# Kernel optimization log

Measured on AMD Instinct MI355X. Metric: run time of the kernel, lower is better.

The kernel has to match this reference:

```python
import jax, jax.numpy as jnp
import numpy as np

NA, NP, NT = 100000, 200000, 50000      # authors, papers, terms
DA, DP, DT = 128, 128, 64               # input feature dims per node type
E_AP, E_PA, E_TP, E_PT = 400000, 400000, 300000, 300000
H, OUT = 64, 4                          # hidden_channels, out_channels
NEG_SLOPE = 0.01                        # nn.LeakyReLU default


def setup_inputs() -> dict:
    keys = iter(jax.random.split(jax.random.key(0), 64))
    rn = lambda shape, s=0.05: jax.random.normal(next(keys), shape, dtype=jnp.float32) * s
    ri = lambda n, hi: jax.random.randint(next(keys), (n,), 0, hi, dtype=jnp.int32)
    inp = {
        'x_author': rn((NA, DA), 1.0),
        'x_paper': rn((NP, DP), 1.0),
        'x_term': rn((NT, DT), 1.0),
        'src_ap': ri(E_AP, NA), 'dst_ap': ri(E_AP, NP),
        'src_pa': ri(E_PA, NP), 'dst_pa': ri(E_PA, NA),
        'src_tp': ri(E_TP, NT), 'dst_tp': ri(E_TP, NP),
        'src_pt': ri(E_PT, NP), 'dst_pt': ri(E_PT, NT),
    }
    # SAGEConv params per edge type: Wl (on mean-aggregated src feats, with bias),
    # Wr (root/dst feats, no bias) -- matches PyG SAGEConv(lin_l, lin_r).
    dims = {'ap': (DA, DP), 'pa': (DP, DA), 'tp': (DT, DP), 'pt': (DP, DT)}
    for et, (ds, dd) in dims.items():
        inp['l1_' + et + '_Wl'] = rn((ds, H))
        inp['l1_' + et + '_bl'] = rn((H,))
        inp['l1_' + et + '_Wr'] = rn((dd, H))
        inp['l2_' + et + '_Wl'] = rn((H, H))
        inp['l2_' + et + '_bl'] = rn((H,))
        inp['l2_' + et + '_Wr'] = rn((H, H))
    inp['lin_W'] = rn((H, OUT))
    inp['lin_b'] = rn((OUT,))
    return inp


def _sage(x_src, x_dst, src, dst, Wl, bl, Wr):
    """PyG SAGEConv (mean aggr): lin_l(mean_j x_src[j]) + lin_r(x_dst)."""
    n_dst = x_dst.shape[0]
    agg = jax.ops.segment_sum(x_src[src], dst, num_segments=n_dst)        # [n_dst, d_src]
    cnt = jax.ops.segment_sum(jnp.ones_like(dst, dtype=x_src.dtype), dst, num_segments=n_dst)
    mean = agg / jnp.maximum(cnt, 1.0)[:, None]
    return mean @ Wl + bl + x_dst @ Wr


def reference(x_author, x_paper, x_term,
              src_ap, dst_ap, src_pa, dst_pa, src_tp, dst_tp, src_pt, dst_pt,
              l1_ap_Wl, l1_ap_bl, l1_ap_Wr, l1_pa_Wl, l1_pa_bl, l1_pa_Wr,
              l1_tp_Wl, l1_tp_bl, l1_tp_Wr, l1_pt_Wl, l1_pt_bl, l1_pt_Wr,
              l2_ap_Wl, l2_ap_bl, l2_ap_Wr, l2_pa_Wl, l2_pa_bl, l2_pa_Wr,
              l2_tp_Wl, l2_tp_bl, l2_tp_Wr, l2_pt_Wl, l2_pt_bl, l2_pt_Wr,
              lin_W, lin_b):
    lrelu = lambda v: jax.nn.leaky_relu(v, NEG_SLOPE)
    # Layer 1 (HeteroConv, sum across relations into each dst type) + LeakyReLU.
    p1 = lrelu(_sage(x_author, x_paper, src_ap, dst_ap, l1_ap_Wl, l1_ap_bl, l1_ap_Wr)
               + _sage(x_term, x_paper, src_tp, dst_tp, l1_tp_Wl, l1_tp_bl, l1_tp_Wr))
    a1 = lrelu(_sage(x_paper, x_author, src_pa, dst_pa, l1_pa_Wl, l1_pa_bl, l1_pa_Wr))
    # (term output of layer 1 / layer-2 paper & term outputs do not reach the
    # returned 'author' logits -- omitted, exactly as autograd would prune them.)
    # Layer 2: author output only needs paper->author relation.
    a2 = _sage(p1, a1, src_pa, dst_pa, l2_pa_Wl, l2_pa_bl, l2_pa_Wr)
    return a2 @ lin_W + lin_b  # [NA, OUT]
```

## Files before the change

### kernel.cpp

```cpp
#include <hip/hip_runtime.h>

#define NA 100000
#define NP 200000
#define NT 50000
#define E_AP 400000
#define E_PA 400000
#define E_TP 300000
#define E_TOT (E_AP + E_TP + E_PA)
#define HD 64
#define NOUT 4
#define NEG 0.01f
#define M_CNT (2 * NP + NA)
#define SCAN_NB ((M_CNT + 1023) / 1024)

typedef __attribute__((ext_vector_type(8))) short bf16x8;
typedef __attribute__((ext_vector_type(4))) float f32x4;

static __device__ __forceinline__ short f2bf(float f) {
  unsigned u = __float_as_uint(f);
  unsigned r = (u + 0x7FFFu + ((u >> 16) & 1u)) >> 16;
  return (short)r;
}
static __device__ __forceinline__ float bflo(unsigned u) {
  return __uint_as_float(u << 16);
}
static __device__ __forceinline__ float bfhi(unsigned u) {
  return __uint_as_float(u & 0xFFFF0000u);
}

static __device__ __forceinline__ void acc8(float* acc, uint4 u, float w) {
  acc[0] = fmaf(w, bflo(u.x), acc[0]);
  acc[1] = fmaf(w, bfhi(u.x), acc[1]);
  acc[2] = fmaf(w, bflo(u.y), acc[2]);
  acc[3] = fmaf(w, bfhi(u.y), acc[3]);
  acc[4] = fmaf(w, bflo(u.z), acc[4]);
  acc[5] = fmaf(w, bfhi(u.z), acc[5]);
  acc[6] = fmaf(w, bflo(u.w), acc[6]);
  acc[7] = fmaf(w, bfhi(u.w), acc[7]);
}

#define R_NP 16384
#define R_NA 32768
#define R_TP 36864
#define R_BLC 36928
#define R_WFL 37184
#define R_WFR 37440
#define R_BF 37444
#define BZ_NB ((M_CNT / 4 + 255) / 256)
__global__ __launch_bounds__(256) void build_zero_kernel(
    const float* __restrict__ l1_ap_Wl, const float* __restrict__ l1_ap_bl,
    const float* __restrict__ l1_ap_Wr,
    const float* __restrict__ l1_pa_Wl, const float* __restrict__ l1_pa_bl,
    const float* __restrict__ l1_pa_Wr,
    const float* __restrict__ l1_tp_Wl, const float* __restrict__ l1_tp_bl,
    const float* __restrict__ l1_tp_Wr,
    const float* __restrict__ l2_Wl, const float* __restrict__ l2_bl,
    const float* __restrict__ l2_Wr,
    const float* __restrict__ lin_W, const float* __restrict__ lin_b,
    short* __restrict__ Wt_np, short* __restrict__ Wt_na, short* __restrict__ Wt_tp,
    float* __restrict__ blc, float* __restrict__ Wfl, float* __restrict__ Wfr,
    float* __restrict__ bf, int* __restrict__ cnt) {
  int t = blockIdx.x * 256 + threadIdx.x;
  int z4 = t * 4;
  if (z4 < M_CNT) *(int4*)(cnt + z4) = make_int4(0, 0, 0, 0);

  if (t < R_NP) {
    int c = t >> 7, k = t & 127;
    float v = (c < 64) ? l1_pa_Wl[k * 64 + c]
                       : (l1_ap_Wr[k * 64 + (c - 64)] + l1_tp_Wr[k * 64 + (c - 64)]);
    Wt_np[t] = f2bf(v);
  } else if (t < R_NA) {
    int i = t - R_NP;
    int c = i >> 7, k = i & 127;
    float v = (c < 64) ? l1_ap_Wl[k * 64 + c] : l1_pa_Wr[k * 64 + (c - 64)];
    Wt_na[i] = f2bf(v);
  } else if (t < R_TP) {
    int i = t - R_NA;
    int c = i >> 6, k = i & 63;
    Wt_tp[i] = f2bf(l1_tp_Wl[k * 64 + c]);
  } else if (t < R_BLC) {
    int c = t - R_TP;
    blc[c] = l1_ap_bl[c] + l1_tp_bl[c];
  } else if (t < R_WFL) {
    int i = t - R_BLC;
    int k = i >> 2, c = i & 3;
    float s = 0.f;
    for (int j = 0; j < HD; ++j) s += l2_Wl[k * HD + j] * lin_W[j * NOUT + c];
    Wfl[i] = s;
  } else if (t < R_WFR) {
    int i = t - R_WFL;
    int k = i >> 2, c = i & 3;
    float s = 0.f;
    for (int j = 0; j < HD; ++j) s += l2_Wr[k * HD + j] * lin_W[j * NOUT + c];
    Wfr[i] = s;
  } else if (t < R_BF) {
    int c = t - R_WFR;
    float s = lin_b[c];
    for (int j = 0; j < HD; ++j) s += l2_bl[j] * lin_W[j * NOUT + c];
    bf[c] = s;
  }
}

__global__ __launch_bounds__(256) void scan1(const int* __restrict__ cnt,
                                             int* __restrict__ offs,
                                             int* __restrict__ bsum) {
  __shared__ int ts[256];
  int t = threadIdx.x;
  int idx = blockIdx.x * 1024 + t * 4;
  int4 v = make_int4(0, 0, 0, 0);
  if (idx < M_CNT) v = *(const int4*)(cnt + idx);
  int s = v.x + v.y + v.z + v.w;
  ts[t] = s;
  __syncthreads();
  for (int off = 1; off < 256; off <<= 1) {
    int a = (t >= off) ? ts[t - off] : 0;
    __syncthreads();
    ts[t] += a;
    __syncthreads();
  }
  int excl = ts[t] - s;
  if (idx < M_CNT) {
    int4 o;
    o.x = excl; o.y = o.x + v.x; o.z = o.y + v.y; o.w = o.z + v.z;
    *(int4*)(offs + idx) = o;
  }
  if (t == 255) bsum[blockIdx.x] = ts[255];
}

__global__ __launch_bounds__(256) void scan2(int* __restrict__ bsum, int nb) {
  __shared__ int ts[256];
  __shared__ int carrysh;
  int t = threadIdx.x;
  int carry = 0;
  for (int base = 0; base < nb; base += 256) {
    int v = (base + t < nb) ? bsum[base + t] : 0;
    ts[t] = v;
    __syncthreads();
    for (int off = 1; off < 256; off <<= 1) {
      int a = (t >= off) ? ts[t - off] : 0;
      __syncthreads();
      ts[t] += a;
      __syncthreads();
    }
    if (base + t < nb) bsum[base + t] = carry + ts[t] - v;
    if (t == 255) carrysh = ts[255];
    __syncthreads();
    carry += carrysh;
    __syncthreads();
  }
}

template <int K, int COLS, bool HAS_OUT1>
static __device__ __forceinline__ void gemm_body(const float* __restrict__ X,
                                                 const short* __restrict__ Wt,
                                                 const float* __restrict__ bias1,
                                                 unsigned short* __restrict__ out0,
                                                 unsigned short* __restrict__ out1,
                                                 int N, int bid,
                                                 unsigned short* __restrict__ lds) {
  constexpr int NSTEP = K / 32;
  constexpr int NTILE = COLS / 16;
  constexpr int WROWB = K * 2;
  constexpr int WBYTES = COLS * K * 2;
  const int t = threadIdx.x;
  const int lane = t & 63;
  const int w = t >> 6;
  const int m = lane & 15;
  const int quad = lane >> 4;

  const int r0 = bid * 128 + w * 16;
  const int r1 = r0 + 64;
  bf16x8 a0[NSTEP], a1[NSTEP];
  {
    const float* x0 = X + (size_t)min(r0 + m, N - 1) * K + quad * 8;
    const float* x1 = X + (size_t)min(r1 + m, N - 1) * K + quad * 8;
#pragma unroll
    for (int s = 0; s < NSTEP; ++s) {
      float4 v0 = *(const float4*)(x0 + s * 32);
      float4 v1 = *(const float4*)(x0 + s * 32 + 4);
      float4 u0 = *(const float4*)(x1 + s * 32);
      float4 u1 = *(const float4*)(x1 + s * 32 + 4);
      bf16x8 a;
      a[0] = f2bf(v0.x); a[1] = f2bf(v0.y); a[2] = f2bf(v0.z); a[3] = f2bf(v0.w);
      a[4] = f2bf(v1.x); a[5] = f2bf(v1.y); a[6] = f2bf(v1.z); a[7] = f2bf(v1.w);
      a0[s] = a;
      bf16x8 b;
      b[0] = f2bf(u0.x); b[1] = f2bf(u0.y); b[2] = f2bf(u0.z); b[3] = f2bf(u0.w);
      b[4] = f2bf(u1.x); b[5] = f2bf(u1.y); b[6] = f2bf(u1.z); b[7] = f2bf(u1.w);
      a1[s] = b;
    }
  }

  {
    const char* wsrc = (const char*)Wt;
    char* wdst = (char*)lds;
#pragma unroll
    for (int i = 0; i < WBYTES / 4096; ++i) {
      const int byte = t * 16 + i * 4096;
      const uint4 v = *(const uint4*)(wsrc + byte);
      const int row = byte / WROWB;
      *(uint4*)(wdst + (byte ^ ((row & 7) << 4))) = v;
    }
  }
  __syncthreads();

  f32x4 acc0[NTILE], acc1[NTILE];
#pragma unroll
  for (int ct = 0; ct < NTILE; ++ct) {
    acc0[ct] = (f32x4){0.f, 0.f, 0.f, 0.f};
    acc1[ct] = (f32x4){0.f, 0.f, 0.f, 0.f};
  }
#pragma unroll
  for (int ct = 0; ct < NTILE; ++ct) {
    const int wrow = ct * 16 + m;
    const int swx = (wrow & 7) << 4;
#pragma unroll
    for (int s = 0; s < NSTEP; ++s) {
      const int byte = wrow * WROWB + s * 64 + quad * 16;
      const bf16x8 b = *(const bf16x8*)((const char*)lds + (byte ^ swx));
      acc0[ct] = __builtin_amdgcn_mfma_f32_16x16x32_bf16(a0[s], b, acc0[ct], 0, 0, 0);
      acc1[ct] = __builtin_amdgcn_mfma_f32_16x16x32_bf16(a1[s], b, acc1[ct], 0, 0, 0);
    }
  }
  __syncthreads();

  constexpr int OROWB = COLS * 2;
#pragma unroll
  for (int ct = 0; ct < NTILE; ++ct) {
    const int col = ct * 16 + m;
    const float add = (HAS_OUT1 && ct >= NTILE / 2) ? bias1[col - 64] : 0.f;
#pragma unroll
    for (int rg = 0; rg < 4; ++rg) {
      const int lr0 = w * 16 + quad * 4 + rg;
      const int lr1 = lr0 + 64;
      const int b0 = lr0 * OROWB + col * 2;
      const int b1 = lr1 * OROWB + col * 2;
      *(unsigned short*)((char*)lds + (b0 ^ ((lr0 & 7) << 4))) =
          (unsigned short)f2bf(acc0[ct][rg] + add);
      *(unsigned short*)((char*)lds + (b1 ^ ((lr1 & 7) << 4))) =
          (unsigned short)f2bf(acc1[ct][rg] + add);
    }
  }
  __syncthreads();

  constexpr int OUTB = 128 * OROWB;
#pragma unroll
  for (int i = 0; i < OUTB / 4096; ++i) {
    const int byte = t * 16 + i * 4096;
    const int row = byte / OROWB;
    const int colb = byte - row * OROWB;
    const uint4 v = *(const uint4*)((const char*)lds + (byte ^ ((row & 7) << 4)));
    const int grow = bid * 128 + row;
    if (grow < N) {
      unsigned short* dst = (HAS_OUT1 && colb >= 128) ? out1 : out0;
      *(uint4*)((char*)dst + (size_t)grow * (HD * 2) + (colb & 127)) = v;
    }
  }
}

#define GB_P ((NP + 127) / 128)
#define GB_A ((NA + 127) / 128)
#define GB_T ((NT + 127) / 128)
#define CNT_NB ((E_TOT / 4 + 255) / 256)

__global__ __launch_bounds__(256, 4) void count_gemm_ta(
    const int* __restrict__ dst_ap, const int* __restrict__ dst_tp,
    const int* __restrict__ dst_pa, int* __restrict__ cnt,
    const float* __restrict__ x_author, const float* __restrict__ x_term,
    const short* __restrict__ Wt_na, const short* __restrict__ Wt_tp,
    const float* __restrict__ l1_pa_bl,
    unsigned short* __restrict__ ya, unsigned short* __restrict__ A1root,
    unsigned short* __restrict__ yt) {
  __shared__ unsigned short lds[16384];
  int b = blockIdx.x;
  if (b < CNT_NB) {
    int i4 = (b * 256 + threadIdx.x) * 4;
    const int* p;
    int base;
    if (i4 < E_AP) { p = dst_ap + i4; base = 0; }
    else if (i4 < E_AP + E_TP) { p = dst_tp + (i4 - E_AP); base = NP; }
    else if (i4 < E_TOT) { p = dst_pa + (i4 - E_AP - E_TP); base = 2 * NP; }
    else return;
    int4 d = *(const int4*)p;
    atomicAdd(&cnt[base + d.x], 1);
    atomicAdd(&cnt[base + d.y], 1);
    atomicAdd(&cnt[base + d.z], 1);
    atomicAdd(&cnt[base + d.w], 1);
  } else if (b < CNT_NB + GB_A) {
    gemm_body<128, 128, true>(x_author, Wt_na, l1_pa_bl, ya, A1root, NA, b - CNT_NB, lds);
  } else {
    gemm_body<64, 64, false>(x_term, Wt_tp, nullptr, yt, nullptr, NT,
                             b - CNT_NB - GB_A, lds);
  }
}

__global__ __launch_bounds__(256, 4) void bucket_gemm_p(
    const int* __restrict__ src_ap, const int* __restrict__ dst_ap,
    const int* __restrict__ src_tp, const int* __restrict__ dst_tp,
    const int* __restrict__ src_pa, const int* __restrict__ dst_pa,
    int* __restrict__ offs, const int* __restrict__ bsum, int* __restrict__ ebuf,
    const float* __restrict__ x_paper, const short* __restrict__ Wt_np,
    const float* __restrict__ blc,
    unsigned short* __restrict__ yp, unsigned short* __restrict__ P1root) {
  __shared__ unsigned short lds[16384];
  int b = blockIdx.x;
  if (b < CNT_NB) {
    int i4 = (b * 256 + threadIdx.x) * 4;
    const int *sp, *dp;
    int base;
    if (i4 < E_AP) { sp = src_ap + i4; dp = dst_ap + i4; base = 0; }
    else if (i4 < E_AP + E_TP) { int j = i4 - E_AP; sp = src_tp + j; dp = dst_tp + j; base = NP; }
    else if (i4 < E_TOT) { int j = i4 - E_AP - E_TP; sp = src_pa + j; dp = dst_pa + j; base = 2 * NP; }
    else return;
    int4 s = *(const int4*)sp;
    int4 d = *(const int4*)dp;
    int gx = base + d.x, gy = base + d.y, gz = base + d.z, gw = base + d.w;
    ebuf[atomicAdd(&offs[gx], 1) + bsum[gx >> 10]] = s.x;
    ebuf[atomicAdd(&offs[gy], 1) + bsum[gy >> 10]] = s.y;
    ebuf[atomicAdd(&offs[gz], 1) + bsum[gz >> 10]] = s.z;
    ebuf[atomicAdd(&offs[gw], 1) + bsum[gw >> 10]] = s.w;
  } else {
    gemm_body<128, 128, true>(x_paper, Wt_np, blc, yp, P1root, NP, b - CNT_NB, lds);
  }
}

__global__ __launch_bounds__(256) void paper_agg(
    const unsigned short* __restrict__ ya, const unsigned short* __restrict__ yt,
    const unsigned short* __restrict__ P1root,
    const int* __restrict__ cnt, const int* __restrict__ offs,
    const int* __restrict__ bsum,
    const int* __restrict__ ebuf, const float* __restrict__ Wfl,
    float* __restrict__ z) {
  const int wv = threadIdx.x >> 6;
  const int lane = threadIdx.x & 63;
  const int g = lane >> 3;
  const int l = lane & 7;
  const int p = blockIdx.x * 32 + wv * 8 + g;
  const bool pv = p < NP;
  const int pc = pv ? p : NP - 1;

  const int cA = cnt[pc], cT = cnt[NP + pc];
  const int startA = offs[pc] + bsum[pc >> 10] - cA;
  const int startT = offs[NP + pc] + bsum[(NP + pc) >> 10] - cT;

  const unsigned short* yab = ya + 8 * l;
  const unsigned short* ytb = yt + 8 * l;

  float accA[8], accT[8];
#pragma unroll
  for (int j = 0; j < 8; ++j) { accA[j] = 0.f; accT[j] = 0.f; }

  const int mx = max(cA, cT);
  for (int i = 0; i < mx; i += 2) {
    const bool a0 = i < cA, a1 = i + 1 < cA;
    const bool t0 = i < cT, t1 = i + 1 < cT;
    int sA0 = ebuf[startA + i];
    int sA1 = ebuf[startA + i + 1];
    int sT0 = ebuf[startT + i];
    int sT1 = ebuf[startT + i + 1];
    sA0 = a0 ? sA0 : 0;
    sA1 = a1 ? sA1 : 0;
    sT0 = t0 ? sT0 : 0;
    sT1 = t1 ? sT1 : 0;
    const uint4 uA0 = *(const uint4*)(yab + (size_t)sA0 * HD);
    const uint4 uA1 = *(const uint4*)(yab + (size_t)sA1 * HD);
    const uint4 uT0 = *(const uint4*)(ytb + (size_t)sT0 * HD);
    const uint4 uT1 = *(const uint4*)(ytb + (size_t)sT1 * HD);
    acc8(accA, uA0, a0 ? 1.f : 0.f);
    acc8(accA, uA1, a1 ? 1.f : 0.f);
    acc8(accT, uT0, t0 ? 1.f : 0.f);
    acc8(accT, uT1, t1 ? 1.f : 0.f);
  }

  const float rA = 1.0f / (float)max(cA, 1);
  const float rT = 1.0f / (float)max(cT, 1);
  uint4 rt = *(const uint4*)(P1root + (size_t)pc * HD + 8 * l);
  float v[8];
  v[0] = bflo(rt.x); v[1] = bfhi(rt.x); v[2] = bflo(rt.y); v[3] = bfhi(rt.y);
  v[4] = bflo(rt.z); v[5] = bfhi(rt.z); v[6] = bflo(rt.w); v[7] = bfhi(rt.w);
  float4 pz = make_float4(0.f, 0.f, 0.f, 0.f);
#pragma unroll
  for (int j = 0; j < 8; ++j) {
    float x = v[j] + accA[j] * rA + accT[j] * rT;
    x = fmaxf(x, NEG * x);
    float4 wf = *(const float4*)(Wfl + (8 * l + j) * 4);
    pz.x += x * wf.x; pz.y += x * wf.y; pz.z += x * wf.z; pz.w += x * wf.w;
  }
#pragma unroll
  for (int m = 1; m < 8; m <<= 1) {
    pz.x += __shfl_xor(pz.x, m);
    pz.y += __shfl_xor(pz.y, m);
    pz.z += __shfl_xor(pz.z, m);
    pz.w += __shfl_xor(pz.w, m);
  }
  if (l == 0 && pv) *(float4*)(z + (size_t)p * NOUT) = pz;
}

__global__ __launch_bounds__(256) void author_agg(
    const unsigned short* __restrict__ yp, const unsigned short* __restrict__ A1root,
    const float* __restrict__ z,
    const int* __restrict__ cnt, const int* __restrict__ offs,
    const int* __restrict__ bsum,
    const int* __restrict__ ebuf, const float* __restrict__ Wfr,
    const float* __restrict__ bf, float* __restrict__ out) {
  const int wv = threadIdx.x >> 6;
  const int lane = threadIdx.x & 63;
  const int g = lane >> 3;
  const int l = lane & 7;
  const int a = blockIdx.x * 32 + wv * 8 + g;
  const bool av = a < NA;
  const int ac = av ? a : NA - 1;

  const int gidx = 2 * NP + ac;
  const int c = cnt[gidx];
  const int start = offs[gidx] + bsum[gidx >> 10] - c;

  const unsigned short* ypb = yp + 8 * l;

  float acc[8];
#pragma unroll
  for (int j = 0; j < 8; ++j) acc[j] = 0.f;
  float4 az = make_float4(0.f, 0.f, 0.f, 0.f);

  for (int i = 0; i < c; i += 2) {
    const bool b1 = i + 1 < c;
    int s0 = ebuf[start + i];
    int s1 = ebuf[min(start + i + 1, E_TOT - 1)];
    s1 = b1 ? s1 : 0;
    const uint4 u0 = *(const uint4*)(ypb + (size_t)s0 * HD);
    const uint4 u1 = *(const uint4*)(ypb + (size_t)s1 * HD);
    const float4 z0 = *(const float4*)(z + (size_t)s0 * NOUT);
    const float4 z1 = *(const float4*)(z + (size_t)s1 * NOUT);
    const float w1 = b1 ? 1.f : 0.f;
    acc8(acc, u0, 1.f);
    acc8(acc, u1, w1);
    az.x = fmaf(w1, z1.x, az.x + z0.x);
    az.y = fmaf(w1, z1.y, az.y + z0.y);
    az.z = fmaf(w1, z1.z, az.z + z0.z);
    az.w = fmaf(w1, z1.w, az.w + z0.w);
  }

  const float r = 1.0f / (float)max(c, 1);
  uint4 rt = *(const uint4*)(A1root + (size_t)ac * HD + 8 * l);
  float v[8];
  v[0] = bflo(rt.x); v[1] = bfhi(rt.x); v[2] = bflo(rt.y); v[3] = bfhi(rt.y);
  v[4] = bflo(rt.z); v[5] = bfhi(rt.z); v[6] = bflo(rt.w); v[7] = bfhi(rt.w);
  float4 o = make_float4(0.f, 0.f, 0.f, 0.f);
#pragma unroll
  for (int j = 0; j < 8; ++j) {
    float x = v[j] + acc[j] * r;
    x = fmaxf(x, NEG * x);
    float4 wf = *(const float4*)(Wfr + (8 * l + j) * 4);
    o.x += x * wf.x; o.y += x * wf.y; o.z += x * wf.z; o.w += x * wf.w;
  }
#pragma unroll
  for (int m = 1; m < 8; m <<= 1) {
    o.x += __shfl_xor(o.x, m);
    o.y += __shfl_xor(o.y, m);
    o.z += __shfl_xor(o.z, m);
    o.w += __shfl_xor(o.w, m);
  }
  if (l == 0 && av) {
    float4 b = *(const float4*)bf;
    o.x += az.x * r + b.x;
    o.y += az.y * r + b.y;
    o.z += az.z * r + b.z;
    o.w += az.w * r + b.w;
    *(float4*)(out + (size_t)a * NOUT) = o;
  }
}

extern "C" void kernel_launch(void* const* d_in, const int* in_sizes, int n_in,
                              void* d_out, int out_size, void* d_ws, size_t ws_size,
                              hipStream_t stream) {
  const float* x_author = (const float*)d_in[0];
  const float* x_paper  = (const float*)d_in[1];
  const float* x_term   = (const float*)d_in[2];
  const int* src_ap = (const int*)d_in[3];
  const int* dst_ap = (const int*)d_in[4];
  const int* src_pa = (const int*)d_in[5];
  const int* dst_pa = (const int*)d_in[6];
  const int* src_tp = (const int*)d_in[7];
  const int* dst_tp = (const int*)d_in[8];
  const float* l1_ap_Wl = (const float*)d_in[11];
  const float* l1_ap_bl = (const float*)d_in[12];
  const float* l1_ap_Wr = (const float*)d_in[13];
  const float* l1_pa_Wl = (const float*)d_in[17];
  const float* l1_pa_bl = (const float*)d_in[18];
  const float* l1_pa_Wr = (const float*)d_in[19];
  const float* l2_pa_Wl = (const float*)d_in[20];
  const float* l2_pa_bl = (const float*)d_in[21];
  const float* l2_pa_Wr = (const float*)d_in[22];
  const float* l1_tp_Wl = (const float*)d_in[23];
  const float* l1_tp_bl = (const float*)d_in[24];
  const float* l1_tp_Wr = (const float*)d_in[25];
  const float* lin_W = (const float*)d_in[35];
  const float* lin_b = (const float*)d_in[36];
  float* out = (float*)d_out;

  char* wsb = (char*)d_ws;
  auto carve = [&](size_t bytes) {
    char* p = wsb;
    wsb += (bytes + 15) & ~(size_t)15;
    return p;
  };
  unsigned short* ya = (unsigned short*)carve((size_t)NA * HD * 2);
  unsigned short* yp = (unsigned short*)carve((size_t)NP * HD * 2);
  unsigned short* yt = (unsigned short*)carve((size_t)NT * HD * 2);
  unsigned short* P1root = (unsigned short*)carve((size_t)NP * HD * 2);
  unsigned short* A1root = (unsigned short*)carve((size_t)NA * HD * 2);
  float* z = (float*)carve((size_t)NP * NOUT * 4);
  int* cnt = (int*)carve((size_t)M_CNT * 4);
  int* offs = (int*)carve((size_t)M_CNT * 4);
  int* bsum = (int*)carve((size_t)SCAN_NB * 4);
  int* ebuf = (int*)carve((size_t)E_TOT * 4);
  short* Wt_np = (short*)carve(128 * 128 * 2);
  short* Wt_na = (short*)carve(128 * 128 * 2);
  short* Wt_tp = (short*)carve(64 * 64 * 2);
  float* blc = (float*)carve(HD * 4);
  float* Wfl = (float*)carve(HD * NOUT * 4);
  float* Wfr = (float*)carve(HD * NOUT * 4);
  float* bf  = (float*)carve(NOUT * 4);

  build_zero_kernel<<<BZ_NB, 256, 0, stream>>>(
      l1_ap_Wl, l1_ap_bl, l1_ap_Wr, l1_pa_Wl, l1_pa_bl, l1_pa_Wr,
      l1_tp_Wl, l1_tp_bl, l1_tp_Wr, l2_pa_Wl, l2_pa_bl, l2_pa_Wr,
      lin_W, lin_b, Wt_np, Wt_na, Wt_tp, blc, Wfl, Wfr, bf, cnt);

  count_gemm_ta<<<CNT_NB + GB_A + GB_T, 256, 0, stream>>>(
      dst_ap, dst_tp, dst_pa, cnt, x_author, x_term, Wt_na, Wt_tp, l1_pa_bl,
      ya, A1root, yt);

  scan1<<<SCAN_NB, 256, 0, stream>>>(cnt, offs, bsum);
  scan2<<<1, 256, 0, stream>>>(bsum, SCAN_NB);

  bucket_gemm_p<<<CNT_NB + GB_P, 256, 0, stream>>>(
      src_ap, dst_ap, src_tp, dst_tp, src_pa, dst_pa, offs, bsum, ebuf,
      x_paper, Wt_np, blc, yp, P1root);

  paper_agg<<<(NP + 31) / 32, 256, 0, stream>>>(ya, yt, P1root, cnt, offs, bsum, ebuf, Wfl, z);
  author_agg<<<(NA + 31) / 32, 256, 0, stream>>>(yp, A1root, z, cnt, offs, bsum, ebuf, Wfr, bf, out);
}
```

Measured before the change: 454.5 us.

## Two-pass binned edge bucketing to localize CSR scatter atomics

Replaces the single-pass random scatter of edges into CSR order with a two-pass scheme. Edges are first coarsely binned by destination range (4096 nodes per bin) using LDS-aggregated bin counters. A second kernel then scatters each bin's edges into ebuf, so atomics and writes stay within a small, cache-resident range. It adds an extra 8-byte-per-edge buffer round trip and a kernel launch, and falls back to the old path if workspace is too small.

After: 480.6 us. +5.7%, slower.

```diff
diff --git a/kernel.cpp b/kernel.cpp
--- a/kernel.cpp
+++ b/kernel.cpp
@@ -12,6 +12,9 @@
 #define NEG 0.01f
 #define M_CNT (2 * NP + NA)
 #define SCAN_NB ((M_CNT + 1023) / 1024)
+#define BINSZ 4096
+#define NBIN ((M_CNT + BINSZ - 1) / BINSZ)
+#define SBPB 8
 
 typedef __attribute__((ext_vector_type(8))) short bf16x8;
 typedef __attribute__((ext_vector_type(4))) float f32x4;
@@ -59,10 +62,11 @@
     const float* __restrict__ lin_W, const float* __restrict__ lin_b,
     short* __restrict__ Wt_np, short* __restrict__ Wt_na, short* __restrict__ Wt_tp,
     float* __restrict__ blc, float* __restrict__ Wfl, float* __restrict__ Wfr,
-    float* __restrict__ bf, int* __restrict__ cnt) {
+    float* __restrict__ bf, int* __restrict__ cnt, int* __restrict__ bincnt) {
   int t = blockIdx.x * 256 + threadIdx.x;
   int z4 = t * 4;
   if (z4 < M_CNT) *(int4*)(cnt + z4) = make_int4(0, 0, 0, 0);
+  if (t < NBIN) bincnt[t] = 0;
 
   if (t < R_NP) {
     int c = t >> 7, k = t & 127;
@@ -127,7 +131,10 @@
   if (t == 255) bsum[blockIdx.x] = ts[255];
 }
 
-__global__ __launch_bounds__(256) void scan2(int* __restrict__ bsum, int nb) {
+__global__ __launch_bounds__(256) void scan2(int* __restrict__ bsum, int nb,
+                                             const int* __restrict__ bincnt,
+                                             int* __restrict__ binoff,
+                                             int* __restrict__ binpos) {
   __shared__ int ts[256];
   __shared__ int carrysh;
   int t = threadIdx.x;
@@ -147,6 +154,20 @@
     __syncthreads();
     carry += carrysh;
     __syncthreads();
+  }
+  int bv = (t < NBIN) ? bincnt[t] : 0;
+  ts[t] = bv;
+  __syncthreads();
+  for (int off = 1; off < 256; off <<= 1) {
+    int a = (t >= off) ? ts[t - off] : 0;
+    __syncthreads();
+    ts[t] += a;
+    __syncthreads();
+  }
+  if (t < NBIN) {
+    int excl = ts[t] - bv;
+    binoff[t] = excl;
+    binpos[t] = excl;
   }
 }
 
@@ -263,9 +284,22 @@
 #define GB_T ((NT + 127) / 128)
 #define CNT_NB ((E_TOT / 4 + 255) / 256)
 
+static __device__ __forceinline__ bool edge_chunk(int i4,
+    const int* __restrict__ src_ap, const int* __restrict__ dst_ap,
+    const int* __restrict__ src_tp, const int* __restrict__ dst_tp,
+    const int* __restrict__ src_pa, const int* __restrict__ dst_pa,
+    const int** sp, const int** dp, int* base) {
+  if (i4 < E_AP) { *sp = src_ap + i4; *dp = dst_ap + i4; *base = 0; return true; }
+  if (i4 < E_AP + E_TP) { int j = i4 - E_AP; *sp = src_tp + j; *dp = dst_tp + j; *base = NP; return true; }
+  if (i4 < E_TOT) { int j = i4 - E_AP - E_TP; *sp = src_pa + j; *dp = dst_pa + j; *base = 2 * NP; return true; }
+  return false;
+}
+
 __global__ __launch_bounds__(256, 4) void count_gemm_ta(
-    const int* __restrict__ dst_ap, const int* __restrict__ dst_tp,
-    const int* __restrict__ dst_pa, int* __restrict__ cnt,
+    const int* __restrict__ src_ap, const int* __restrict__ dst_ap,
+    const int* __restrict__ src_tp, const int* __restrict__ dst_tp,
+    const int* __restrict__ src_pa, const int* __restrict__ dst_pa,
+    int* __restrict__ cnt, int* __restrict__ bincnt,
     const float* __restrict__ x_author, const float* __restrict__ x_term,
     const short* __restrict__ Wt_na, const short* __restrict__ Wt_tp,
     const float* __restrict__ l1_pa_bl,
@@ -274,23 +308,94 @@
   __shared__ unsigned short lds[16384];
   int b = blockIdx.x;
   if (b < CNT_NB) {
+    int* lbin = (int*)lds;
+    for (int i = threadIdx.x; i < NBIN; i += 256) lbin[i] = 0;
+    __syncthreads();
     int i4 = (b * 256 + threadIdx.x) * 4;
-    const int* p;
+    const int *sp, *dp;
     int base;
-    if (i4 < E_AP) { p = dst_ap + i4; base = 0; }
-    else if (i4 < E_AP + E_TP) { p = dst_tp + (i4 - E_AP); base = NP; }
-    else if (i4 < E_TOT) { p = dst_pa + (i4 - E_AP - E_TP); base = 2 * NP; }
-    else return;
-    int4 d = *(const int4*)p;
-    atomicAdd(&cnt[base + d.x], 1);
-    atomicAdd(&cnt[base + d.y], 1);
-    atomicAdd(&cnt[base + d.z], 1);
-    atomicAdd(&cnt[base + d.w], 1);
+    if (edge_chunk(i4, src_ap, dst_ap, src_tp, dst_tp, src_pa, dst_pa, &sp, &dp, &base)) {
+      int4 d = *(const int4*)dp;
+      int gx = base + d.x, gy = base + d.y, gz = base + d.z, gw = base + d.w;
+      atomicAdd(&cnt[gx], 1); atomicAdd(&lbin[gx >> 12], 1);
+      atomicAdd(&cnt[gy], 1); atomicAdd(&lbin[gy >> 12], 1);
+      atomicAdd(&cnt[gz], 1); atomicAdd(&lbin[gz >> 12], 1);
+      atomicAdd(&cnt[gw], 1); atomicAdd(&lbin[gw >> 12], 1);
+    }
+    __syncthreads();
+    for (int i = threadIdx.x; i < NBIN; i += 256)
+      if (lbin[i]) atomicAdd(&bincnt[i], lbin[i]);
   } else if (b < CNT_NB + GB_A) {
     gemm_body<128, 128, true>(x_author, Wt_na, l1_pa_bl, ya, A1root, NA, b - CNT_NB, lds);
   } else {
     gemm_body<64, 64, false>(x_term, Wt_tp, nullptr, yt, nullptr, NT,
                              b - CNT_NB - GB_A, lds);
+  }
+}
+
+__global__ __launch_bounds__(256, 4) void append_gemm_p(
+    const int* __restrict__ src_ap, const int* __restrict__ dst_ap,
+    const int* __restrict__ src_tp, const int* __restrict__ dst_tp,
+    const int* __restrict__ src_pa, const int* __restrict__ dst_pa,
+    int* __restrict__ binpos, int2* __restrict__ binbuf,
+    const float* __restrict__ x_paper, const short* __restrict__ Wt_np,
+    const float* __restrict__ blc,
+    unsigned short* __restrict__ yp, unsigned short* __restrict__ P1root) {
+  __shared__ unsigned short lds[16384];
+  int b = blockIdx.x;
+  if (b < CNT_NB) {
+    int* lcnt = (int*)lds;
+    int* lbase = lcnt + NBIN;
+    for (int i = threadIdx.x; i < NBIN; i += 256) lcnt[i] = 0;
+    __syncthreads();
+    int i4 = (b * 256 + threadIdx.x) * 4;
+    const int *sp, *dp;
+    int base;
+    int bins[4], lidx[4], srcs[4], gs[4];
+    bool valid = edge_chunk(i4, src_ap, dst_ap, src_tp, dst_tp, src_pa, dst_pa,
+                            &sp, &dp, &base);
+    if (valid) {
+      int4 s = *(const int4*)sp;
+      int4 d = *(const int4*)dp;
+      srcs[0] = s.x; srcs[1] = s.y; srcs[2] = s.z; srcs[3] = s.w;
+      gs[0] = base + d.x; gs[1] = base + d.y; gs[2] = base + d.z; gs[3] = base + d.w;
+#pragma unroll
+      for (int k = 0; k < 4; ++k) {
+        bins[k] = gs[k] >> 12;
+        lidx[k] = atomicAdd(&lcnt[bins[k]], 1);
+      }
+    }
+    __syncthreads();
+    for (int i = threadIdx.x; i < NBIN; i += 256)
+      lbase[i] = lcnt[i] ? atomicAdd(&binpos[i], lcnt[i]) : 0;
+    __syncthreads();
+    if (valid) {
+#pragma unroll
+      for (int k = 0; k < 4; ++k)
+        binbuf[lbase[bins[k]] + lidx[k]] = make_int2(srcs[k], gs[k]);
+    }
+  } else {
+    gemm_body<128, 128, true>(x_paper, Wt_np, blc, yp, P1root, NP, b - CNT_NB, lds);
+  }
+}
+
+__global__ __launch_bounds__(256) void scatter_kernel(
+    const int* __restrict__ binoff, const int* __restrict__ binpos,
+    const int2* __restrict__ binbuf,
+    int* __restrict__ offs, const int* __restrict__ bsum,
+    int* __restrict__ ebuf) {
+  const int bin = blockIdx.x / SBPB;
+  const int part = blockIdx.x % SBPB;
+  const int start = binoff[bin];
+  const int end = binpos[bin];
+  for (int idx = start + part * 1024 + threadIdx.x * 4; idx < end; idx += SBPB * 1024) {
+#pragma unroll
+    for (int k = 0; k < 4; ++k) {
+      if (idx + k < end) {
+        int2 p = binbuf[idx + k];
+        ebuf[atomicAdd(&offs[p.y], 1) + bsum[p.y >> 10]] = p.x;
+      }
+    }
   }
 }
 
@@ -308,10 +413,8 @@
     int i4 = (b * 256 + threadIdx.x) * 4;
     const int *sp, *dp;
     int base;
-    if (i4 < E_AP) { sp = src_ap + i4; dp = dst_ap + i4; base = 0; }
-    else if (i4 < E_AP + E_TP) { int j = i4 - E_AP; sp = src_tp + j; dp = dst_tp + j; base = NP; }
-    else if (i4 < E_TOT) { int j = i4 - E_AP - E_TP; sp = src_pa + j; dp = dst_pa + j; base = 2 * NP; }
-    else return;
+    if (!edge_chunk(i4, src_ap, dst_ap, src_tp, dst_tp, src_pa, dst_pa, &sp, &dp, &base))
+      return;
     int4 s = *(const int4*)sp;
     int4 d = *(const int4*)dp;
     int gx = base + d.x, gy = base + d.y, gz = base + d.z, gw = base + d.w;
@@ -521,22 +624,36 @@
   float* Wfl = (float*)carve(HD * NOUT * 4);
   float* Wfr = (float*)carve(HD * NOUT * 4);
   float* bf  = (float*)carve(NOUT * 4);
+  int* bincnt = (int*)carve(NBIN * 4);
+  int* binoff = (int*)carve(NBIN * 4);
+  int* binpos = (int*)carve(NBIN * 4);
+  size_t used = (size_t)(wsb - (char*)d_ws);
+  bool two_pass = (ws_size >= used + (size_t)E_TOT * 8 + 64);
+  int2* binbuf = two_pass ? (int2*)carve((size_t)E_TOT * 8) : nullptr;
 
   build_zero_kernel<<<BZ_NB, 256, 0, stream>>>(
       l1_ap_Wl, l1_ap_bl, l1_ap_Wr, l1_pa_Wl, l1_pa_bl, l1_pa_Wr,
       l1_tp_Wl, l1_tp_bl, l1_tp_Wr, l2_pa_Wl, l2_pa_bl, l2_pa_Wr,
-      lin_W, lin_b, Wt_np, Wt_na, Wt_tp, blc, Wfl, Wfr, bf, cnt);
+      lin_W, lin_b, Wt_np, Wt_na, Wt_tp, blc, Wfl, Wfr, bf, cnt, bincnt);
 
   count_gemm_ta<<<CNT_NB + GB_A + GB_T, 256, 0, stream>>>(
-      dst_ap, dst_tp, dst_pa, cnt, x_author, x_term, Wt_na, Wt_tp, l1_pa_bl,
-      ya, A1root, yt);
+      src_ap, dst_ap, src_tp, dst_tp, src_pa, dst_pa, cnt, bincnt,
+      x_author, x_term, Wt_na, Wt_tp, l1_pa_bl, ya, A1root, yt);
 
   scan1<<<SCAN_NB, 256, 0, stream>>>(cnt, offs, bsum);
-  scan2<<<1, 256, 0, stream>>>(bsum, SCAN_NB);
-
-  bucket_gemm_p<<<CNT_NB + GB_P, 256, 0, stream>>>(
-      src_ap, dst_ap, src_tp, dst_tp, src_pa, dst_pa, offs, bsum, ebuf,
-      x_paper, Wt_np, blc, yp, P1root);
+  scan2<<<1, 256, 0, stream>>>(bsum, SCAN_NB, bincnt, binoff, binpos);
+
+  if (two_pass) {
+    append_gemm_p<<<CNT_NB + GB_P, 256, 0, stream>>>(
+        src_ap, dst_ap, src_tp, dst_tp, src_pa, dst_pa, binpos, binbuf,
+        x_paper, Wt_np, blc, yp, P1root);
+    scatter_kernel<<<NBIN * SBPB, 256, 0, stream>>>(binoff, binpos, binbuf,
+                                                    offs, bsum, ebuf);
+  } else {
+    bucket_gemm_p<<<CNT_NB + GB_P, 256, 0, stream>>>(
+        src_ap, dst_ap, src_tp, dst_tp, src_pa, dst_pa, offs, bsum, ebuf,
+        x_paper, Wt_np, blc, yp, P1root);
+  }
 
   paper_agg<<<(NP + 31) / 32, 256, 0, stream>>>(ya, yt, P1root, cnt, offs, bsum, ebuf, Wfl, z);
   author_agg<<<(NA + 31) / 32, 256, 0, stream>>>(yp, A1root, z, cnt, offs, bsum, ebuf, Wfr, bf, out);
```
